# Performance work log

Measured on AMD Instinct MI355X. Metric: run time of the kernel, lower is better.

## Reference

```python
import jax, jax.numpy as jnp
import numpy as np

B, L, D = 8, 4096, 256
G, K = 64, 8          # n_groups, group_size
N = G * K             # 512 slots
H = 8                 # attention heads
EPS = 1e-5

def _ln(x, g, b):
    m = jnp.mean(x, axis=-1, keepdims=True)
    v = jnp.var(x, axis=-1, keepdims=True)
    return (x - m) * jax.lax.rsqrt(v + EPS) * g + b

def _gelu(x):
    return jax.nn.gelu(x, approximate=False)  # torch nn.GELU default = exact erf

def setup_inputs() -> dict:
    key = jax.random.key(0)
    ks = jax.random.split(key, 24)
    s = 0.02
    d = {
        'X': jax.random.normal(ks[0], (B, L, D), jnp.float32),
        'S': jax.random.normal(ks[1], (B, N, D), jnp.float32),
        'Wg':  jax.random.normal(ks[2], (D, G)) * s,
        'Wk':  jax.random.normal(ks[3], (D, K)) * s,
        'Wm1': jax.random.normal(ks[4], (D, 2*D)) * s, 'bm1': jnp.zeros((2*D,)),
        'Wm2': jax.random.normal(ks[5], (2*D, D)) * s, 'bm2': jnp.zeros((D,)),
        'Wgt1': jax.random.normal(ks[6], (D, D)) * s, 'bgt1': jnp.zeros((D,)),
        'Wgt2': jax.random.normal(ks[7], (D, 1)) * s, 'bgt2': jnp.zeros((1,)),
        'Wqkv': jax.random.normal(ks[8], (D, 3*D)) * s, 'bqkv': jnp.zeros((3*D,)),
        'Wo':  jax.random.normal(ks[9], (D, D)) * s, 'bo': jnp.zeros((D,)),
        'aln_g': jnp.ones((D,)), 'aln_b': jnp.zeros((D,)),
        'Wu1': jax.random.normal(ks[10], (2*D, 2*D)) * s, 'bu1': jnp.zeros((2*D,)),
        'Wu2': jax.random.normal(ks[11], (2*D, D)) * s, 'bu2': jnp.zeros((D,)),
        'ln_g': jnp.ones((D,)), 'ln_b': jnp.zeros((D,)),
    }
    return d

def reference(X, S, Wg, Wk, Wm1, bm1, Wm2, bm2, Wgt1, bgt1, Wgt2, bgt2,
              Wqkv, bqkv, Wo, bo, aln_g, aln_b, Wu1, bu1, Wu2, bu2, ln_g, ln_b):
    # --- hierarchical routing (eval path: argmax one-hot) ---
    msg = _gelu(X @ Wm1 + bm1) @ Wm2 + bm2                 # (B,L,D)
    gate = jax.nn.sigmoid(_gelu(X @ Wgt1 + bgt1) @ Wgt2 + bgt2)  # (B,L,1)
    gm = msg * gate
    gidx = jnp.argmax(X @ Wg, axis=-1)                     # (B,L)
    kidx = jnp.argmax(X @ Wk, axis=-1)                     # (B,L)
    idx = gidx * K + kidx                                  # flat slot id in [0,N)
    full = jax.nn.one_hot(idx, N, dtype=X.dtype)           # (B,L,N)
    incoming = jnp.einsum('bln,bld->bnd', full, gm)        # (B,N,D)
    # --- slot self-attention ---
    qkv = S @ Wqkv + bqkv
    q, k, v = jnp.split(qkv, 3, axis=-1)
    dh = D // H
    q = q.reshape(B, N, H, dh); k = k.reshape(B, N, H, dh); v = v.reshape(B, N, H, dh)
    scores = jnp.einsum('bqhd,bkhd->bhqk', q, k) / jnp.sqrt(jnp.asarray(dh, X.dtype))
    attn = jax.nn.softmax(scores, axis=-1)
    o = jnp.einsum('bhqk,bkhd->bqhd', attn, v).reshape(B, N, D) @ Wo + bo
    S1 = _ln(S + o, aln_g, aln_b)
    # --- update ---
    cat = jnp.concatenate([S1, incoming], axis=-1)         # (B,N,2D)
    S2 = S1 + _gelu(cat @ Wu1 + bu1) @ Wu2 + bu2
    return _ln(S2, ln_g, ln_b)
```

## Files before the change

### kernel.cpp

```cpp
#include <hip/hip_runtime.h>

typedef __bf16 bf16_t;
typedef __bf16 bf16x8 __attribute__((ext_vector_type(8)));
typedef __bf16 bf16x4v __attribute__((ext_vector_type(4)));
typedef __bf16 bf16x2v __attribute__((ext_vector_type(2)));
typedef float f32x4 __attribute__((ext_vector_type(4)));
typedef unsigned long long u64;

#define LN_EPS 1e-5f

__device__ __forceinline__ float erf_fast(float a) {
  const float t = fabsf(a);
  const float s = a * a;
  float r;
  if (t > 0.921875f) {
    float u;
    r = fmaf(-1.72853470e-5f, t, 3.83197126e-4f);
    u = fmaf(-3.88396438e-3f, t, 2.42546219e-2f);
    r = fmaf(r, s, u);
    r = fmaf(r, t, 1.06777877e-1f);
    r = fmaf(r, t, -6.37245935e-1f);
    r = fmaf(r, t, -1.28717512e-1f);
    r = fmaf(r, t, t);
    r = 1.0f - __expf(-r);
    r = copysignf(r, a);
  } else {
    r = -5.96761703e-4f;
    r = fmaf(r, s, 4.99119423e-3f);
    r = fmaf(r, s, -2.67681349e-2f);
    r = fmaf(r, s, 1.12819925e-1f);
    r = fmaf(r, s, -3.76125336e-1f);
    r = fmaf(r, s, 1.28379166e-1f);
    r = fmaf(r, a, a);
  }
  return r;
}

__device__ __forceinline__ float gelu_f(float x) {
  const float h = 0.5f * x;
  return fmaf(h, erf_fast(x * 0.70710678118654752f), h);
}

__device__ __forceinline__ void async16(const bf16_t* g, bf16_t* l) {
  __builtin_amdgcn_global_load_lds(
      (const __attribute__((address_space(1))) void*)g,
      (__attribute__((address_space(3))) void*)l, 16, 0, 0);
}

__global__ __launch_bounds__(256)
void prep_kernel(const float* __restrict__ X, const float* __restrict__ S,
                 const float* __restrict__ Wg, const float* __restrict__ Wk,
                 const float* __restrict__ Wm1, const float* __restrict__ Wgt1,
                 const float* __restrict__ Wm2, const float* __restrict__ Wqkv,
                 const float* __restrict__ Wo, const float* __restrict__ Wu1,
                 const float* __restrict__ Wu2,
                 bf16_t* __restrict__ Xb, bf16_t* __restrict__ Sb,
                 bf16_t* __restrict__ W1t, bf16_t* __restrict__ W2t,
                 bf16_t* __restrict__ Wqkvt, bf16_t* __restrict__ Wot,
                 bf16_t* __restrict__ Wu1t, bf16_t* __restrict__ Wu2t,
                 float4* __restrict__ zbase)
{
  const int bid = blockIdx.x;
  const int t = threadIdx.x;
  if (bid < 8192) {
    const int i = bid * 256 + t;
    const float4 v = ((const float4*)X)[i];
    bf16x4v o; o[0]=(bf16_t)v.x; o[1]=(bf16_t)v.y; o[2]=(bf16_t)v.z; o[3]=(bf16_t)v.w;
    ((bf16x4v*)Xb)[i] = o;
  } else if (bid < 9216) {
    const int i = (bid - 8192) * 256 + t;
    const float4 v = ((const float4*)S)[i];
    bf16x4v o; o[0]=(bf16_t)v.x; o[1]=(bf16_t)v.y; o[2]=(bf16_t)v.z; o[3]=(bf16_t)v.w;
    ((bf16x4v*)Sb)[i] = o;
  } else if (bid < 10112) {
    const int n = bid - 9216;
    const int k = t;
    float v;
    if (n < 512)      v = Wm1[k * 512 + n];
    else if (n < 768) v = Wgt1[k * 256 + (n - 512)];
    else if (n < 832) v = Wg[k * 64 + (n - 768)];
    else if (n < 840) v = Wk[k * 8 + (n - 832)];
    else              v = 0.f;
    W1t[n * 256 + k] = (bf16_t)v;
  } else if (bid < 10368) {
    const int n = bid - 10112;
    for (int k = t; k < 512; k += 256) W2t[n * 512 + k] = (bf16_t)Wm2[k * 256 + n];
  } else if (bid < 11136) {
    const int n = bid - 10368;
    Wqkvt[n * 256 + t] = (bf16_t)Wqkv[t * 768 + n];
  } else if (bid < 11392) {
    const int n = bid - 11136;
    Wot[n * 256 + t] = (bf16_t)Wo[t * 256 + n];
  } else if (bid < 11904) {
    const int n = bid - 11392;
    for (int k = t; k < 512; k += 256) Wu1t[n * 512 + k] = (bf16_t)Wu1[k * 512 + n];
  } else if (bid < 12160) {
    const int n = bid - 11904;
    for (int k = t; k < 512; k += 256) Wu2t[n * 512 + k] = (bf16_t)Wu2[k * 256 + n];
  } else {
    zbase[(bid - 12160) * 256 + t] = make_float4(0.f, 0.f, 0.f, 0.f);
  }
}

__global__ __launch_bounds__(256, 2)
void g1_kernel(const bf16_t* __restrict__ A,
               const bf16_t* __restrict__ Bt,
               const float* __restrict__ bias, const float* __restrict__ bias2,
               bf16_t* __restrict__ h1,
               const float* __restrict__ wgt2, float* __restrict__ gatelin,
               u64* __restrict__ bitmap)
{
  const int m0 = blockIdx.x * 128;
  const int by = blockIdx.y;
  const int n0 = by * 128;
  const int t = threadIdx.x;
  const int w = t >> 6;
  const int lane = t & 63;
  const int wr = w >> 1, wc = w & 1;
  const int quad = lane >> 4, l15 = lane & 15;

  __shared__ bf16_t lA[128 * 32];
  __shared__ bf16_t lB[128 * 32];
  __shared__ float sWg[256];
  __shared__ int sKi[128];

  if (by >= 4 && by < 6) sWg[t] = wgt2[t];

  f32x4 acc[4][4];
#pragma unroll
  for (int mt = 0; mt < 4; ++mt)
#pragma unroll
    for (int nt = 0; nt < 4; ++nt)
      acc[mt][nt] = (f32x4){0.f, 0.f, 0.f, 0.f};

  const int srow = t >> 2;
  const int schunk = ((t & 3) ^ (srow & 3)) * 8;
  const int ko = ((quad ^ (l15 & 3)) << 3);

  for (int k0 = 0; k0 < 256; k0 += 32) {
#pragma unroll
    for (int i = 0; i < 2; ++i) {
      const int row = i * 64 + srow;
      async16(A + (size_t)(m0 + row) * 256 + k0 + schunk,
              lA + (size_t)(i * 256 + (t & 192)) * 8);
      async16(Bt + (size_t)(n0 + row) * 256 + k0 + schunk,
              lB + (size_t)(i * 256 + (t & 192)) * 8);
    }
    __syncthreads();
    bf16x8 af[4], bfr[4];
#pragma unroll
    for (int mt = 0; mt < 4; ++mt)
      af[mt] = *(const bf16x8*)&lA[(wr * 64 + mt * 16 + l15) * 32 + ko];
#pragma unroll
    for (int nt = 0; nt < 4; ++nt)
      bfr[nt] = *(const bf16x8*)&lB[(wc * 64 + nt * 16 + l15) * 32 + ko];
#pragma unroll
    for (int mt = 0; mt < 4; ++mt)
#pragma unroll
      for (int nt = 0; nt < 4; ++nt)
        acc[mt][nt] = __builtin_amdgcn_mfma_f32_16x16x32_bf16(bfr[nt], af[mt], acc[mt][nt], 0, 0, 0);
    __syncthreads();
  }

  if (by < 4) {
#pragma unroll
    for (int mt = 0; mt < 4; ++mt) {
      const int row = m0 + wr * 64 + mt * 16 + l15;
#pragma unroll
      for (int nt = 0; nt < 4; ++nt) {
        const int colb = n0 + wc * 64 + nt * 16 + quad * 4;
        const float4 bb = *(const float4*)&bias[colb];
        bf16x4v o;
        o[0] = (bf16_t)gelu_f(acc[mt][nt][0] + bb.x);
        o[1] = (bf16_t)gelu_f(acc[mt][nt][1] + bb.y);
        o[2] = (bf16_t)gelu_f(acc[mt][nt][2] + bb.z);
        o[3] = (bf16_t)gelu_f(acc[mt][nt][3] + bb.w);
        *(bf16x4v*)&h1[(size_t)row * 512 + colb] = o;
      }
    }
  } else if (by < 6) {
#pragma unroll
    for (int mt = 0; mt < 4; ++mt) {
      const int row = m0 + wr * 64 + mt * 16 + l15;
      float part = 0.f;
#pragma unroll
      for (int nt = 0; nt < 4; ++nt) {
        const int colb = n0 + wc * 64 + nt * 16 + quad * 4;
        const int c = colb - 512;
        const float4 bb = *(const float4*)&bias2[c];
        part = fmaf(gelu_f(acc[mt][nt][0] + bb.x), sWg[c + 0], part);
        part = fmaf(gelu_f(acc[mt][nt][1] + bb.y), sWg[c + 1], part);
        part = fmaf(gelu_f(acc[mt][nt][2] + bb.z), sWg[c + 2], part);
        part = fmaf(gelu_f(acc[mt][nt][3] + bb.w), sWg[c + 3], part);
      }
      part += __shfl_xor(part, 16, 64);
      part += __shfl_xor(part, 32, 64);
      if (lane < 16) atomicAdd(&gatelin[row], part);
    }
  } else {
    int bi[4];
#pragma unroll
    for (int mt = 0; mt < 4; ++mt) {
      if (wc == 0) {
        float mv = -1e30f; int mi = 0;
#pragma unroll
        for (int nt = 0; nt < 4; ++nt)
#pragma unroll
          for (int j = 0; j < 4; ++j) {
            const int gc = nt * 16 + quad * 4 + j;
            const float v = acc[mt][nt][j];
            if (v > mv || (v == mv && gc < mi)) { mv = v; mi = gc; }
          }
#pragma unroll
        for (int off = 16; off <= 32; off <<= 1) {
          const float ov = __shfl_xor(mv, off, 64);
          const int oi = __shfl_xor(mi, off, 64);
          if (ov > mv || (ov == mv && oi < mi)) { mv = ov; mi = oi; }
        }
        bi[mt] = mi;
      } else {
        float mv = -1e30f; int mi = 0;
        if (quad < 2) {
#pragma unroll
          for (int j = 0; j < 4; ++j) {
            const int kc = quad * 4 + j;
            const float v = acc[mt][0][j];
            if (v > mv || (v == mv && kc < mi)) { mv = v; mi = kc; }
          }
        }
#pragma unroll
        for (int off = 16; off <= 32; off <<= 1) {
          const float ov = __shfl_xor(mv, off, 64);
          const int oi = __shfl_xor(mi, off, 64);
          if (ov > mv || (ov == mv && oi < mi)) { mv = ov; mi = oi; }
        }
        if (lane < 16) sKi[wr * 64 + mt * 16 + l15] = mi;
      }
    }
    __syncthreads();
    if (wc == 0 && lane < 16) {
#pragma unroll
      for (int mt = 0; mt < 4; ++mt) {
        const int rl = wr * 64 + mt * 16 + l15;
        const int row = m0 + rl;
        const int idx = bi[mt] * 8 + sKi[rl];
        const int b = row >> 12, tok = row & 4095;
        atomicOr(&bitmap[(size_t)(b * 512 + idx) * 64 + (tok >> 6)],
                 1ull << (tok & 63));
      }
    }
  }
}

template<int MT, int EPI>
__global__ __launch_bounds__(256)
void gemm_kernel(const bf16_t* __restrict__ A, int lda,
                 const bf16_t* __restrict__ Bt, int K,
                 const float* __restrict__ bias, const float* __restrict__ bias2,
                 void* __restrict__ outp, int ldc,
                 const float* __restrict__ wgt2, float* __restrict__ gatelin,
                 u64* __restrict__ bitmap)
{
  constexpr int BM = MT * 32;
  constexpr int CA = BM * 4;
  const int m0 = blockIdx.x * BM;
  const int by = blockIdx.y;
  const int n0 = by * 128;
  const int t = threadIdx.x;
  const int w = t >> 6;
  const int lane = t & 63;
  const int wr = w >> 1, wc = w & 1;
  const int quad = lane >> 4, l15 = lane & 15;

  __shared__ bf16_t lA[BM * 32];
  __shared__ bf16_t lB[128 * 32];

  f32x4 acc[MT][4];
#pragma unroll
  for (int mt = 0; mt < MT; ++mt)
#pragma unroll
    for (int nt = 0; nt < 4; ++nt)
      acc[mt][nt] = (f32x4){0.f, 0.f, 0.f, 0.f};

  for (int k0 = 0; k0 < K; k0 += 32) {
    if constexpr (CA >= 256) {
#pragma unroll
      for (int i = 0; i < CA / 256; ++i) {
        const int c = i * 256 + t;
        async16(A + (size_t)(m0 + (c >> 2)) * lda + k0 + (c & 3) * 8,
                lA + (size_t)(i * 256 + (t & 192)) * 8);
      }
    } else {
      if (t < CA)
        async16(A + (size_t)(m0 + (t >> 2)) * lda + k0 + (t & 3) * 8,
                lA + (size_t)(t & 192) * 8);
    }
#pragma unroll
    for (int i = 0; i < 2; ++i) {
      const int c = i * 256 + t;
      async16(Bt + (size_t)(n0 + (c >> 2)) * K + k0 + (c & 3) * 8,
              lB + (size_t)(i * 256 + (t & 192)) * 8);
    }
    __syncthreads();
    bf16x8 af[MT], bfr[4];
    const int ko = quad * 8;
#pragma unroll
    for (int mt = 0; mt < MT; ++mt)
      af[mt] = *(const bf16x8*)&lA[(wr * MT * 16 + mt * 16 + l15) * 32 + ko];
#pragma unroll
    for (int nt = 0; nt < 4; ++nt)
      bfr[nt] = *(const bf16x8*)&lB[(wc * 64 + nt * 16 + l15) * 32 + ko];
#pragma unroll
    for (int mt = 0; mt < MT; ++mt)
#pragma unroll
      for (int nt = 0; nt < 4; ++nt)
        acc[mt][nt] = __builtin_amdgcn_mfma_f32_16x16x32_bf16(bfr[nt], af[mt], acc[mt][nt], 0, 0, 0);
    __syncthreads();
  }

#pragma unroll
  for (int mt = 0; mt < MT; ++mt) {
    const int row = m0 + wr * MT * 16 + mt * 16 + l15;
#pragma unroll
    for (int nt = 0; nt < 4; ++nt) {
      const int colb = n0 + wc * 64 + nt * 16 + quad * 4;
      const float4 bb = *(const float4*)&bias[colb];
      bf16x4v o;
      o[0]=(bf16_t)gelu_f(acc[mt][nt][0]+bb.x); o[1]=(bf16_t)gelu_f(acc[mt][nt][1]+bb.y);
      o[2]=(bf16_t)gelu_f(acc[mt][nt][2]+bb.z); o[3]=(bf16_t)gelu_f(acc[mt][nt][3]+bb.w);
      *(bf16x4v*)&((bf16_t*)outp)[(size_t)row * ldc + colb] = o;
    }
  }
  (void)bias2; (void)wgt2; (void)gatelin; (void)bitmap;
}

__global__ __launch_bounds__(256)
void gemm_pair_kernel(const bf16_t* __restrict__ H, const bf16_t* __restrict__ W2t,
                      const float* __restrict__ bm2, const float* __restrict__ sumg,
                      float* __restrict__ incom,
                      const bf16_t* __restrict__ Sb, const bf16_t* __restrict__ Wqkvt,
                      const float* __restrict__ bqkv, bf16_t* __restrict__ qkvb,
                      bf16_t* __restrict__ Vt)
{
  int id = blockIdx.x;
  const bool first = id < 256;
  if (!first) id -= 256;
  const bf16_t* A  = first ? H : Sb;
  const bf16_t* Bt = first ? W2t : Wqkvt;
  const float* bias = first ? bm2 : bqkv;
  const int lda = first ? 512 : 256;
  const int K   = first ? 512 : 256;
  const int ldc = first ? 256 : 768;
  const int m0 = (id & 127) * 32;
  const int n0 = (id >> 7) * 128;
  const int t = threadIdx.x;
  const int w = t >> 6;
  const int lane = t & 63;
  const int wr = w >> 1, wc = w & 1;
  const int quad = lane >> 4, l15 = lane & 15;

  __shared__ bf16_t lA[32 * 32];
  __shared__ bf16_t lB[128 * 32];

  f32x4 acc[4];
#pragma unroll
  for (int nt = 0; nt < 4; ++nt) acc[nt] = (f32x4){0.f, 0.f, 0.f, 0.f};

  for (int k0 = 0; k0 < K; k0 += 32) {
    if (t < 128)
      async16(A + (size_t)(m0 + (t >> 2)) * lda + k0 + (t & 3) * 8,
              lA + (size_t)(t & 192) * 8);
#pragma unroll
    for (int i = 0; i < 2; ++i) {
      const int c = i * 256 + t;
      async16(Bt + (size_t)(n0 + (c >> 2)) * K + k0 + (c & 3) * 8,
              lB + (size_t)(i * 256 + (t & 192)) * 8);
    }
    __syncthreads();
    bf16x8 af, bfr[4];
    const int ko = quad * 8;
    af = *(const bf16x8*)&lA[(wr * 16 + l15) * 32 + ko];
#pragma unroll
    for (int nt = 0; nt < 4; ++nt)
      bfr[nt] = *(const bf16x8*)&lB[(wc * 64 + nt * 16 + l15) * 32 + ko];
#pragma unroll
    for (int nt = 0; nt < 4; ++nt)
      acc[nt] = __builtin_amdgcn_mfma_f32_16x16x32_bf16(bfr[nt], af, acc[nt], 0, 0, 0);
    __syncthreads();
  }

  const int row = m0 + wr * 16 + l15;
  if (first) {
    const float gt = sumg[row];
#pragma unroll
    for (int nt = 0; nt < 4; ++nt) {
      const int colb = n0 + wc * 64 + nt * 16 + quad * 4;
      const float4 bb = *(const float4*)&bias[colb];
      *(float4*)&incom[(size_t)row * ldc + colb] =
          make_float4(fmaf(gt, bb.x, acc[nt][0]), fmaf(gt, bb.y, acc[nt][1]),
                      fmaf(gt, bb.z, acc[nt][2]), fmaf(gt, bb.w, acc[nt][3]));
    }
  } else if (n0 < 512) {
#pragma unroll
    for (int nt = 0; nt < 4; ++nt) {
      const int colb = n0 + wc * 64 + nt * 16 + quad * 4;
      const float4 bb = *(const float4*)&bias[colb];
      bf16x4v o; o[0]=(bf16_t)(acc[nt][0]+bb.x); o[1]=(bf16_t)(acc[nt][1]+bb.y);
      o[2]=(bf16_t)(acc[nt][2]+bb.z); o[3]=(bf16_t)(acc[nt][3]+bb.w);
      *(bf16x4v*)&qkvb[(size_t)row * ldc + colb] = o;
    }
  } else {
    const int b = row >> 9, key = row & 511;
#pragma unroll
    for (int nt = 0; nt < 4; ++nt) {
      const int colb = n0 + wc * 64 + nt * 16 + quad * 4;
      const int c = colb - 512;
      const int h2 = c >> 5, dh = c & 31;
      const float4 bb = *(const float4*)&bias[colb];
      bf16_t* vb = Vt + ((size_t)(b * 8 + h2) * 32 + dh) * 512 + key;
      vb[0]   = (bf16_t)(acc[nt][0] + bb.x);
      vb[512] = (bf16_t)(acc[nt][1] + bb.y);
      vb[1024]= (bf16_t)(acc[nt][2] + bb.z);
      vb[1536]= (bf16_t)(acc[nt][3] + bb.w);
    }
  }
}

__global__ __launch_bounds__(256)
void gather_kernel(const bf16_t* __restrict__ h1, const float* __restrict__ gatelin,
                   const float* __restrict__ bgt2, const u64* __restrict__ bitmap,
                   bf16_t* __restrict__ H, float* __restrict__ sumg)
{
  const int bs = blockIdx.x;
  const int b = bs >> 9;
  const int t = threadIdx.x;
  __shared__ u64 sw[64];
  if (t < 64) sw[t] = bitmap[(size_t)bs * 64 + t];
  __syncthreads();
  const float bg = bgt2[0];
  float a0 = 0.f, a1 = 0.f, sg = 0.f;
  for (int wd = 0; wd < 64; ++wd) {
    u64 word = sw[wd];
    while (word) {
      const int bit = __builtin_ctzll(word);
      word &= word - 1;
      const int l = (b << 12) + (wd << 6) + bit;
      const float g = 1.0f / (1.0f + __expf(-(gatelin[l] + bg)));
      const bf16x2v hv = *(const bf16x2v*)&h1[(size_t)l * 512 + t * 2];
      a0 = fmaf(g, (float)hv[0], a0);
      a1 = fmaf(g, (float)hv[1], a1);
      sg += g;
    }
  }
  bf16x2v o; o[0] = (bf16_t)a0; o[1] = (bf16_t)a1;
  *(bf16x2v*)&H[(size_t)bs * 512 + t * 2] = o;
  if (t == 0) sumg[bs] = sg;
}

__global__ __launch_bounds__(256)
void attn_kernel(const bf16_t* __restrict__ qkv, const bf16_t* __restrict__ Vt,
                 bf16_t* __restrict__ obuf)
{
  const int bid = blockIdx.x;
  const int qc = bid & 15;
  const int h = (bid >> 4) & 7;
  const int b = bid >> 7;
  const int t = threadIdx.x;
  const int w = t >> 6, lane = t & 63;
  const int quad = lane >> 4, l15 = lane & 15;

  __shared__ bf16_t sP[32 * 520];
  __shared__ float sL[32];

  bf16x8 qf[2];
#pragma unroll
  for (int mt = 0; mt < 2; ++mt) {
    const int row = b * 512 + qc * 32 + mt * 16 + l15;
    qf[mt] = *(const bf16x8*)&qkv[(size_t)row * 768 + h * 32 + quad * 8];
  }
  const float scale = 0.17677669529663687f;
  for (int kt = w; kt < 32; kt += 4) {
    const int key = b * 512 + kt * 16 + l15;
    const bf16x8 kf = *(const bf16x8*)&qkv[(size_t)key * 768 + 256 + h * 32 + quad * 8];
#pragma unroll
    for (int mt = 0; mt < 2; ++mt) {
      f32x4 c = (f32x4){0.f, 0.f, 0.f, 0.f};
      c = __builtin_amdgcn_mfma_f32_16x16x32_bf16(qf[mt], kf, c, 0, 0, 0);
#pragma unroll
      for (int r = 0; r < 4; ++r)
        sP[(mt * 16 + quad * 4 + r) * 520 + kt * 16 + l15] = (bf16_t)(c[r] * scale);
    }
  }
  __syncthreads();

#pragma unroll
  for (int ri = 0; ri < 8; ++ri) {
    const int row = w * 8 + ri;
    const bf16x8 sv = *(const bf16x8*)&sP[row * 520 + lane * 8];
    float sval[8];
    float mx = -1e30f;
#pragma unroll
    for (int j = 0; j < 8; ++j) { sval[j] = (float)sv[j]; mx = fmaxf(mx, sval[j]); }
#pragma unroll
    for (int off = 32; off; off >>= 1) mx = fmaxf(mx, __shfl_xor(mx, off, 64));
    float sum = 0.f;
    bf16x8 pv;
#pragma unroll
    for (int j = 0; j < 8; ++j) { const float e = __expf(sval[j] - mx); sum += e; pv[j] = (bf16_t)e; }
#pragma unroll
    for (int off = 32; off; off >>= 1) sum += __shfl_xor(sum, off, 64);
    *(bf16x8*)&sP[row * 520 + lane * 8] = pv;
    if (lane == 0) sL[row] = sum;
  }
  __syncthreads();

  const int wq = w >> 1, wd = w & 1;
  const bf16_t* vbase = Vt + ((size_t)(b * 8 + h) * 32 + wd * 16 + l15) * 512;
  const bf16_t* pbase = &sP[(wq * 16 + l15) * 520];
  f32x4 oacc = (f32x4){0.f, 0.f, 0.f, 0.f};
#pragma unroll
  for (int kt = 0; kt < 16; ++kt) {
    const bf16x8 af = *(const bf16x8*)&pbase[kt * 32 + quad * 8];
    const bf16x8 vf = *(const bf16x8*)&vbase[kt * 32 + quad * 8];
    oacc = __builtin_amdgcn_mfma_f32_16x16x32_bf16(vf, af, oacc, 0, 0, 0);
  }
  const int rowq = wq * 16 + l15;
  const float inv = 1.0f / sL[rowq];
  bf16x4v o;
#pragma unroll
  for (int r = 0; r < 4; ++r) o[r] = (bf16_t)(oacc[r] * inv);
  *(bf16x4v*)&obuf[(size_t)(b * 512 + qc * 32 + rowq) * 256 + h * 32 + wd * 16 + quad * 4] = o;
}

__global__ __launch_bounds__(256)
void wo_ln1_kernel(const bf16_t* __restrict__ obuf, const bf16_t* __restrict__ Wot,
                   const float* __restrict__ bo, const float* __restrict__ S,
                   const float* __restrict__ incom, const float* __restrict__ g,
                   const float* __restrict__ bb, float* __restrict__ S1f,
                   bf16_t* __restrict__ A4)
{
  const int m0 = blockIdx.x * 16;
  const int t = threadIdx.x;
  const int w = t >> 6, lane = t & 63;
  const int quad = lane >> 4, l15 = lane & 15;

  __shared__ bf16_t lA[16 * 32];
  __shared__ bf16_t lB[256 * 32];
  __shared__ float sSum[4][16];
  __shared__ float sSq[4][16];

  f32x4 acc[4];
#pragma unroll
  for (int nt = 0; nt < 4; ++nt) acc[nt] = (f32x4){0.f, 0.f, 0.f, 0.f};

  for (int k0 = 0; k0 < 256; k0 += 32) {
    if (t < 64)
      async16(obuf + (size_t)(m0 + (t >> 2)) * 256 + k0 + (t & 3) * 8, lA);
#pragma unroll
    for (int i = 0; i < 4; ++i) {
      const int c = i * 256 + t;
      async16(Wot + (size_t)(c >> 2) * 256 + k0 + (c & 3) * 8,
              lB + (size_t)(i * 256 + (t & 192)) * 8);
    }
    __syncthreads();
    const int ko = quad * 8;
    const bf16x8 af = *(const bf16x8*)&lA[l15 * 32 + ko];
#pragma unroll
    for (int nt = 0; nt < 4; ++nt) {
      const bf16x8 bfr = *(const bf16x8*)&lB[(w * 64 + nt * 16 + l15) * 32 + ko];
      acc[nt] = __builtin_amdgcn_mfma_f32_16x16x32_bf16(bfr, af, acc[nt], 0, 0, 0);
    }
    __syncthreads();
  }

  const int row = m0 + l15;
  float sum = 0.f, sq = 0.f;
#pragma unroll
  for (int nt = 0; nt < 4; ++nt) {
    const int colb = w * 64 + nt * 16 + quad * 4;
    const float4 bv = *(const float4*)&bo[colb];
    const float4 sv = *(const float4*)&S[(size_t)row * 256 + colb];
    float x0 = acc[nt][0] + bv.x + sv.x, x1 = acc[nt][1] + bv.y + sv.y;
    float x2 = acc[nt][2] + bv.z + sv.z, x3 = acc[nt][3] + bv.w + sv.w;
    acc[nt][0] = x0; acc[nt][1] = x1; acc[nt][2] = x2; acc[nt][3] = x3;
    sum += x0 + x1 + x2 + x3;
    sq += x0*x0 + x1*x1 + x2*x2 + x3*x3;
  }
  sum += __shfl_xor(sum, 16, 64); sum += __shfl_xor(sum, 32, 64);
  sq  += __shfl_xor(sq, 16, 64);  sq  += __shfl_xor(sq, 32, 64);
  if (lane < 16) { sSum[w][l15] = sum; sSq[w][l15] = sq; }
  __syncthreads();
  const float tot = sSum[0][l15] + sSum[1][l15] + sSum[2][l15] + sSum[3][l15];
  const float tq  = sSq[0][l15] + sSq[1][l15] + sSq[2][l15] + sSq[3][l15];
  const float mean = tot * 0.00390625f;
  const float var = tq * 0.00390625f - mean * mean;
  const float rstd = rsqrtf(var + LN_EPS);
#pragma unroll
  for (int nt = 0; nt < 4; ++nt) {
    const int colb = w * 64 + nt * 16 + quad * 4;
    const float4 gg = *(const float4*)&g[colb];
    const float4 bv = *(const float4*)&bb[colb];
    const float y0 = (acc[nt][0]-mean)*rstd*gg.x + bv.x;
    const float y1 = (acc[nt][1]-mean)*rstd*gg.y + bv.y;
    const float y2 = (acc[nt][2]-mean)*rstd*gg.z + bv.z;
    const float y3 = (acc[nt][3]-mean)*rstd*gg.w + bv.w;
    *(float4*)&S1f[(size_t)row * 256 + colb] = make_float4(y0, y1, y2, y3);
    bf16x4v yb; yb[0]=(bf16_t)y0; yb[1]=(bf16_t)y1; yb[2]=(bf16_t)y2; yb[3]=(bf16_t)y3;
    *(bf16x4v*)&A4[(size_t)row * 512 + colb] = yb;
    const float4 ic = *(const float4*)&incom[(size_t)row * 256 + colb];
    bf16x4v ib; ib[0]=(bf16_t)ic.x; ib[1]=(bf16_t)ic.y; ib[2]=(bf16_t)ic.z; ib[3]=(bf16_t)ic.w;
    *(bf16x4v*)&A4[(size_t)row * 512 + 256 + colb] = ib;
  }
}

__global__ __launch_bounds__(256)
void wu2_ln2_kernel(const bf16_t* __restrict__ U, const bf16_t* __restrict__ Wu2t,
                    const float* __restrict__ bu2, const float* __restrict__ S1f,
                    const float* __restrict__ g, const float* __restrict__ bb,
                    float* __restrict__ out)
{
  const int m0 = blockIdx.x * 16;
  const int t = threadIdx.x;
  const int w = t >> 6, lane = t & 63;
  const int quad = lane >> 4, l15 = lane & 15;

  __shared__ bf16_t lA[16 * 32];
  __shared__ bf16_t lB[256 * 32];
  __shared__ float sSum[4][16];
  __shared__ float sSq[4][16];

  f32x4 acc[4];
#pragma unroll
  for (int nt = 0; nt < 4; ++nt) acc[nt] = (f32x4){0.f, 0.f, 0.f, 0.f};

  for (int k0 = 0; k0 < 512; k0 += 32) {
    if (t < 64)
      async16(U + (size_t)(m0 + (t >> 2)) * 512 + k0 + (t & 3) * 8, lA);
#pragma unroll
    for (int i = 0; i < 4; ++i) {
      const int c = i * 256 + t;
      async16(Wu2t + (size_t)(c >> 2) * 512 + k0 + (c & 3) * 8,
              lB + (size_t)(i * 256 + (t & 192)) * 8);
    }
    __syncthreads();
    const int ko = quad * 8;
    const bf16x8 af = *(const bf16x8*)&lA[l15 * 32 + ko];
#pragma unroll
    for (int nt = 0; nt < 4; ++nt) {
      const bf16x8 bfr = *(const bf16x8*)&lB[(w * 64 + nt * 16 + l15) * 32 + ko];
      acc[nt] = __builtin_amdgcn_mfma_f32_16x16x32_bf16(bfr, af, acc[nt], 0, 0, 0);
    }
    __syncthreads();
  }

  const int row = m0 + l15;
  float sum = 0.f, sq = 0.f;
#pragma unroll
  for (int nt = 0; nt < 4; ++nt) {
    const int colb = w * 64 + nt * 16 + quad * 4;
    const float4 bv = *(const float4*)&bu2[colb];
    const float4 sv = *(const float4*)&S1f[(size_t)row * 256 + colb];
    float x0 = acc[nt][0] + bv.x + sv.x, x1 = acc[nt][1] + bv.y + sv.y;
    float x2 = acc[nt][2] + bv.z + sv.z, x3 = acc[nt][3] + bv.w + sv.w;
    acc[nt][0] = x0; acc[nt][1] = x1; acc[nt][2] = x2; acc[nt][3] = x3;
    sum += x0 + x1 + x2 + x3;
    sq += x0*x0 + x1*x1 + x2*x2 + x3*x3;
  }
  sum += __shfl_xor(sum, 16, 64); sum += __shfl_xor(sum, 32, 64);
  sq  += __shfl_xor(sq, 16, 64);  sq  += __shfl_xor(sq, 32, 64);
  if (lane < 16) { sSum[w][l15] = sum; sSq[w][l15] = sq; }
  __syncthreads();
  const float tot = sSum[0][l15] + sSum[1][l15] + sSum[2][l15] + sSum[3][l15];
  const float tq  = sSq[0][l15] + sSq[1][l15] + sSq[2][l15] + sSq[3][l15];
  const float mean = tot * 0.00390625f;
  const float var = tq * 0.00390625f - mean * mean;
  const float rstd = rsqrtf(var + LN_EPS);
#pragma unroll
  for (int nt = 0; nt < 4; ++nt) {
    const int colb = w * 64 + nt * 16 + quad * 4;
    const float4 gg = *(const float4*)&g[colb];
    const float4 bv = *(const float4*)&bb[colb];
    *(float4*)&out[(size_t)row * 256 + colb] = make_float4(
        (acc[nt][0]-mean)*rstd*gg.x + bv.x, (acc[nt][1]-mean)*rstd*gg.y + bv.y,
        (acc[nt][2]-mean)*rstd*gg.z + bv.z, (acc[nt][3]-mean)*rstd*gg.w + bv.w);
  }
}

extern "C" void kernel_launch(void* const* d_in, const int* in_sizes, int n_in,
                              void* d_out, int out_size, void* d_ws, size_t ws_size,
                              hipStream_t stream)
{
  (void)in_sizes; (void)n_in; (void)out_size; (void)ws_size;
  const float* X    = (const float*)d_in[0];
  const float* S    = (const float*)d_in[1];
  const float* Wg   = (const float*)d_in[2];
  const float* Wk   = (const float*)d_in[3];
  const float* Wm1  = (const float*)d_in[4];
  const float* bm1  = (const float*)d_in[5];
  const float* Wm2  = (const float*)d_in[6];
  const float* bm2  = (const float*)d_in[7];
  const float* Wgt1 = (const float*)d_in[8];
  const float* bgt1 = (const float*)d_in[9];
  const float* Wgt2 = (const float*)d_in[10];
  const float* bgt2 = (const float*)d_in[11];
  const float* Wqkv = (const float*)d_in[12];
  const float* bqkv = (const float*)d_in[13];
  const float* Wo   = (const float*)d_in[14];
  const float* bo   = (const float*)d_in[15];
  const float* alng = (const float*)d_in[16];
  const float* alnb = (const float*)d_in[17];
  const float* Wu1  = (const float*)d_in[18];
  const float* bu1  = (const float*)d_in[19];
  const float* Wu2  = (const float*)d_in[20];
  const float* bu2  = (const float*)d_in[21];
  const float* lng  = (const float*)d_in[22];
  const float* lnb  = (const float*)d_in[23];

  char* p = (char*)d_ws;
  auto carve = [&](size_t bytes) { char* r = p; p += bytes; return r; };
  bf16_t* Xb    = (bf16_t*)carve(16777216);
  bf16_t* Sb    = (bf16_t*)carve(2097152);
  bf16_t* W1t   = (bf16_t*)carve(458752);
  bf16_t* W2t   = (bf16_t*)carve(262144);
  bf16_t* Wqkvt = (bf16_t*)carve(393216);
  bf16_t* Wot   = (bf16_t*)carve(131072);
  bf16_t* Wu1t  = (bf16_t*)carve(524288);
  bf16_t* Wu2t  = (bf16_t*)carve(262144);
  bf16_t* h1    = (bf16_t*)carve(33554432);
  u64*    bitmap  = (u64*)carve(2097152);
  float*  gatelin = (float*)carve(131072);
  float*  incom = (float*)carve(4194304);
  bf16_t* qkvb  = (bf16_t*)carve(6291456);
  bf16_t* Vt    = (bf16_t*)carve(2097152);
  bf16_t* obuf  = (bf16_t*)carve(2097152);
  float*  S1f   = (float*)carve(4194304);
  bf16_t* A4    = (bf16_t*)carve(4194304);
  bf16_t* U     = (bf16_t*)carve(4194304);
  float*  sumg  = (float*)carve(16384);
  bf16_t* H = U;

  prep_kernel<<<12704, 256, 0, stream>>>(X, S, Wg, Wk, Wm1, Wgt1, Wm2, Wqkv, Wo, Wu1, Wu2,
                                         Xb, Sb, W1t, W2t, Wqkvt, Wot, Wu1t, Wu2t,
                                         (float4*)bitmap);
  g1_kernel<<<dim3(256, 7), 256, 0, stream>>>(Xb, W1t, bm1, bgt1, h1,
                                              Wgt2, gatelin, bitmap);
  gather_kernel<<<4096, 256, 0, stream>>>(h1, gatelin, bgt2, bitmap, H, sumg);
  gemm_pair_kernel<<<1024, 256, 0, stream>>>(H, W2t, bm2, sumg, incom,
                                             Sb, Wqkvt, bqkv, qkvb, Vt);
  attn_kernel<<<1024, 256, 0, stream>>>(qkvb, Vt, obuf);
  wo_ln1_kernel<<<256, 256, 0, stream>>>(obuf, Wot, bo, S, incom, alng, alnb, S1f, A4);
  gemm_kernel<2,5><<<dim3(64,4), 256, 0, stream>>>(A4, 512, Wu1t, 512, bu1, nullptr, U, 512,
                                                   nullptr, nullptr, nullptr);
  wu2_ln2_kernel<<<256, 256, 0, stream>>>(U, Wu2t, bu2, S1f, lng, lnb, (float*)d_out);
}
```

Measured before the change: 254.8 us.

## Double-buffer LDS in GEMM kernels and enlarge pair/Wu1 tiles to 128x128

Adds double-buffered shared-memory staging so the async global loads for the next K slice overlap the MFMA work on the current one, with one barrier per slice, in g1, the QKV/W2 pair GEMM and the Wu1 GEMM. The pair and Wu1 GEMMs move from 32- and 64-row tiles to 128x128 tiles with the XOR-swizzled LDS layout, which gives more data reuse per block. The trade-off is far fewer blocks: 256 for the pair kernel and 128 for Wu1 on a GPU with many CUs, which risks leaving compute units idle. It also doubles LDS use per block.

```diff
diff --git a/kernel.cpp b/kernel.cpp
--- a/kernel.cpp
+++ b/kernel.cpp
@@ -119,8 +119,8 @@
   const int wr = w >> 1, wc = w & 1;
   const int quad = lane >> 4, l15 = lane & 15;
 
-  __shared__ bf16_t lA[128 * 32];
-  __shared__ bf16_t lB[128 * 32];
+  __shared__ bf16_t lA[2][128 * 32];
+  __shared__ bf16_t lB[2][128 * 32];
   __shared__ float sWg[256];
   __shared__ int sKi[128];
 
@@ -136,29 +136,40 @@
   const int srow = t >> 2;
   const int schunk = ((t & 3) ^ (srow & 3)) * 8;
   const int ko = ((quad ^ (l15 & 3)) << 3);
-
-  for (int k0 = 0; k0 < 256; k0 += 32) {
+  const int ldst = (t & 192) * 8;
+
+  auto STAGE = [&](int buf, int k0) {
 #pragma unroll
     for (int i = 0; i < 2; ++i) {
       const int row = i * 64 + srow;
-      async16(A + (size_t)(m0 + row) * 256 + k0 + schunk,
-              lA + (size_t)(i * 256 + (t & 192)) * 8);
-      async16(Bt + (size_t)(n0 + row) * 256 + k0 + schunk,
-              lB + (size_t)(i * 256 + (t & 192)) * 8);
-    }
-    __syncthreads();
+      async16(A + (size_t)(m0 + row) * 256 + k0 + schunk, &lA[buf][i * 2048 + ldst]);
+      async16(Bt + (size_t)(n0 + row) * 256 + k0 + schunk, &lB[buf][i * 2048 + ldst]);
+    }
+  };
+  auto COMPUTE = [&](int buf) {
     bf16x8 af[4], bfr[4];
 #pragma unroll
     for (int mt = 0; mt < 4; ++mt)
-      af[mt] = *(const bf16x8*)&lA[(wr * 64 + mt * 16 + l15) * 32 + ko];
+      af[mt] = *(const bf16x8*)&lA[buf][(wr * 64 + mt * 16 + l15) * 32 + ko];
 #pragma unroll
     for (int nt = 0; nt < 4; ++nt)
-      bfr[nt] = *(const bf16x8*)&lB[(wc * 64 + nt * 16 + l15) * 32 + ko];
+      bfr[nt] = *(const bf16x8*)&lB[buf][(wc * 64 + nt * 16 + l15) * 32 + ko];
 #pragma unroll
     for (int mt = 0; mt < 4; ++mt)
 #pragma unroll
       for (int nt = 0; nt < 4; ++nt)
         acc[mt][nt] = __builtin_amdgcn_mfma_f32_16x16x32_bf16(bfr[nt], af[mt], acc[mt][nt], 0, 0, 0);
+  };
+
+  STAGE(0, 0);
+  __syncthreads();
+#pragma unroll
+  for (int k0 = 0; k0 < 256; k0 += 64) {
+    STAGE(1, k0 + 32);
+    COMPUTE(0);
+    __syncthreads();
+    if (k0 + 64 < 256) STAGE(0, k0 + 64);
+    COMPUTE(1);
     __syncthreads();
   }
 
@@ -252,75 +263,191 @@
   }
 }
 
-template<int MT, int EPI>
-__global__ __launch_bounds__(256)
-void gemm_kernel(const bf16_t* __restrict__ A, int lda,
-                 const bf16_t* __restrict__ Bt, int K,
-                 const float* __restrict__ bias, const float* __restrict__ bias2,
-                 void* __restrict__ outp, int ldc,
-                 const float* __restrict__ wgt2, float* __restrict__ gatelin,
-                 u64* __restrict__ bitmap)
-{
-  constexpr int BM = MT * 32;
-  constexpr int CA = BM * 4;
-  const int m0 = blockIdx.x * BM;
-  const int by = blockIdx.y;
-  const int n0 = by * 128;
+__global__ __launch_bounds__(256, 2)
+void pair128_kernel(const bf16_t* __restrict__ H, const bf16_t* __restrict__ W2t,
+                    const float* __restrict__ bm2, const float* __restrict__ sumg,
+                    float* __restrict__ incom,
+                    const bf16_t* __restrict__ Sb, const bf16_t* __restrict__ Wqkvt,
+                    const float* __restrict__ bqkv, bf16_t* __restrict__ qkvb,
+                    bf16_t* __restrict__ Vt)
+{
+  int id = blockIdx.x;
+  const bool first = id < 64;
+  if (!first) id -= 64;
+  const bf16_t* A  = first ? H : Sb;
+  const bf16_t* Bt = first ? W2t : Wqkvt;
+  const float* bias = first ? bm2 : bqkv;
+  const int lda = first ? 512 : 256;
+  const int K   = first ? 512 : 256;
+  const int m0 = (id & 31) * 128;
+  const int n0 = (id >> 5) * 128;
   const int t = threadIdx.x;
   const int w = t >> 6;
   const int lane = t & 63;
   const int wr = w >> 1, wc = w & 1;
   const int quad = lane >> 4, l15 = lane & 15;
 
-  __shared__ bf16_t lA[BM * 32];
-  __shared__ bf16_t lB[128 * 32];
-
-  f32x4 acc[MT][4];
-#pragma unroll
-  for (int mt = 0; mt < MT; ++mt)
+  __shared__ bf16_t lA[2][128 * 32];
+  __shared__ bf16_t lB[2][128 * 32];
+
+  f32x4 acc[4][4];
+#pragma unroll
+  for (int mt = 0; mt < 4; ++mt)
 #pragma unroll
     for (int nt = 0; nt < 4; ++nt)
       acc[mt][nt] = (f32x4){0.f, 0.f, 0.f, 0.f};
 
-  for (int k0 = 0; k0 < K; k0 += 32) {
-    if constexpr (CA >= 256) {
-#pragma unroll
-      for (int i = 0; i < CA / 256; ++i) {
-        const int c = i * 256 + t;
-        async16(A + (size_t)(m0 + (c >> 2)) * lda + k0 + (c & 3) * 8,
-                lA + (size_t)(i * 256 + (t & 192)) * 8);
-      }
-    } else {
-      if (t < CA)
-        async16(A + (size_t)(m0 + (t >> 2)) * lda + k0 + (t & 3) * 8,
-                lA + (size_t)(t & 192) * 8);
-    }
+  const int srow = t >> 2;
+  const int schunk = ((t & 3) ^ (srow & 3)) * 8;
+  const int ko = ((quad ^ (l15 & 3)) << 3);
+  const int ldst = (t & 192) * 8;
+
+  auto STAGE = [&](int buf, int k0) {
 #pragma unroll
     for (int i = 0; i < 2; ++i) {
-      const int c = i * 256 + t;
-      async16(Bt + (size_t)(n0 + (c >> 2)) * K + k0 + (c & 3) * 8,
-              lB + (size_t)(i * 256 + (t & 192)) * 8);
-    }
-    __syncthreads();
-    bf16x8 af[MT], bfr[4];
-    const int ko = quad * 8;
-#pragma unroll
-    for (int mt = 0; mt < MT; ++mt)
-      af[mt] = *(const bf16x8*)&lA[(wr * MT * 16 + mt * 16 + l15) * 32 + ko];
+      const int row = i * 64 + srow;
+      async16(A + (size_t)(m0 + row) * lda + k0 + schunk, &lA[buf][i * 2048 + ldst]);
+      async16(Bt + (size_t)(n0 + row) * K + k0 + schunk, &lB[buf][i * 2048 + ldst]);
+    }
+  };
+  auto COMPUTE = [&](int buf) {
+    bf16x8 af[4], bfr[4];
+#pragma unroll
+    for (int mt = 0; mt < 4; ++mt)
+      af[mt] = *(const bf16x8*)&lA[buf][(wr * 64 + mt * 16 + l15) * 32 + ko];
 #pragma unroll
     for (int nt = 0; nt < 4; ++nt)
-      bfr[nt] = *(const bf16x8*)&lB[(wc * 64 + nt * 16 + l15) * 32 + ko];
-#pragma unroll
-    for (int mt = 0; mt < MT; ++mt)
+      bfr[nt] = *(const bf16x8*)&lB[buf][(wc * 64 + nt * 16 + l15) * 32 + ko];
+#pragma unroll
+    for (int mt = 0; mt < 4; ++mt)
 #pragma unroll
       for (int nt = 0; nt < 4; ++nt)
         acc[mt][nt] = __builtin_amdgcn_mfma_f32_16x16x32_bf16(bfr[nt], af[mt], acc[mt][nt], 0, 0, 0);
-    __syncthreads();
-  }
-
-#pragma unroll
-  for (int mt = 0; mt < MT; ++mt) {
-    const int row = m0 + wr * MT * 16 + mt * 16 + l15;
+  };
+
+  STAGE(0, 0);
+  __syncthreads();
+  for (int k0 = 0; k0 < K; k0 += 64) {
+    STAGE(1, k0 + 32);
+    COMPUTE(0);
+    __syncthreads();
+    if (k0 + 64 < K) STAGE(0, k0 + 64);
+    COMPUTE(1);
+    __syncthreads();
+  }
+
+  if (first) {
+#pragma unroll
+    for (int mt = 0; mt < 4; ++mt) {
+      const int row = m0 + wr * 64 + mt * 16 + l15;
+      const float gt = sumg[row];
+#pragma unroll
+      for (int nt = 0; nt < 4; ++nt) {
+        const int colb = n0 + wc * 64 + nt * 16 + quad * 4;
+        const float4 bb = *(const float4*)&bias[colb];
+        *(float4*)&incom[(size_t)row * 256 + colb] =
+            make_float4(fmaf(gt, bb.x, acc[mt][nt][0]), fmaf(gt, bb.y, acc[mt][nt][1]),
+                        fmaf(gt, bb.z, acc[mt][nt][2]), fmaf(gt, bb.w, acc[mt][nt][3]));
+      }
+    }
+  } else if (n0 < 512) {
+#pragma unroll
+    for (int mt = 0; mt < 4; ++mt) {
+      const int row = m0 + wr * 64 + mt * 16 + l15;
+#pragma unroll
+      for (int nt = 0; nt < 4; ++nt) {
+        const int colb = n0 + wc * 64 + nt * 16 + quad * 4;
+        const float4 bb = *(const float4*)&bias[colb];
+        bf16x4v o; o[0]=(bf16_t)(acc[mt][nt][0]+bb.x); o[1]=(bf16_t)(acc[mt][nt][1]+bb.y);
+        o[2]=(bf16_t)(acc[mt][nt][2]+bb.z); o[3]=(bf16_t)(acc[mt][nt][3]+bb.w);
+        *(bf16x4v*)&qkvb[(size_t)row * 768 + colb] = o;
+      }
+    }
+  } else {
+#pragma unroll
+    for (int mt = 0; mt < 4; ++mt) {
+      const int row = m0 + wr * 64 + mt * 16 + l15;
+      const int b = row >> 9, key = row & 511;
+#pragma unroll
+      for (int nt = 0; nt < 4; ++nt) {
+        const int colb = n0 + wc * 64 + nt * 16 + quad * 4;
+        const int c = colb - 512;
+        const int h2 = c >> 5, dh = c & 31;
+        const float4 bb = *(const float4*)&bias[colb];
+        bf16_t* vb = Vt + ((size_t)(b * 8 + h2) * 32 + dh) * 512 + key;
+        vb[0]   = (bf16_t)(acc[mt][nt][0] + bb.x);
+        vb[512] = (bf16_t)(acc[mt][nt][1] + bb.y);
+        vb[1024]= (bf16_t)(acc[mt][nt][2] + bb.z);
+        vb[1536]= (bf16_t)(acc[mt][nt][3] + bb.w);
+      }
+    }
+  }
+}
+
+__global__ __launch_bounds__(256, 2)
+void g128_gelu_kernel(const bf16_t* __restrict__ A, const bf16_t* __restrict__ Bt,
+                      const float* __restrict__ bias, bf16_t* __restrict__ out)
+{
+  const int m0 = blockIdx.x * 128;
+  const int n0 = blockIdx.y * 128;
+  const int t = threadIdx.x;
+  const int w = t >> 6;
+  const int lane = t & 63;
+  const int wr = w >> 1, wc = w & 1;
+  const int quad = lane >> 4, l15 = lane & 15;
+
+  __shared__ bf16_t lA[2][128 * 32];
+  __shared__ bf16_t lB[2][128 * 32];
+
+  f32x4 acc[4][4];
+#pragma unroll
+  for (int mt = 0; mt < 4; ++mt)
+#pragma unroll
+    for (int nt = 0; nt < 4; ++nt)
+      acc[mt][nt] = (f32x4){0.f, 0.f, 0.f, 0.f};
+
+  const int srow = t >> 2;
+  const int schunk = ((t & 3) ^ (srow & 3)) * 8;
+  const int ko = ((quad ^ (l15 & 3)) << 3);
+  const int ldst = (t & 192) * 8;
+
+  auto STAGE = [&](int buf, int k0) {
+#pragma unroll
+    for (int i = 0; i < 2; ++i) {
+      const int row = i * 64 + srow;
+      async16(A + (size_t)(m0 + row) * 512 + k0 + schunk, &lA[buf][i * 2048 + ldst]);
+      async16(Bt + (size_t)(n0 + row) * 512 + k0 + schunk, &lB[buf][i * 2048 + ldst]);
+    }
+  };
+  auto COMPUTE = [&](int buf) {
+    bf16x8 af[4], bfr[4];
+#pragma unroll
+    for (int mt = 0; mt < 4; ++mt)
+      af[mt] = *(const bf16x8*)&lA[buf][(wr * 64 + mt * 16 + l15) * 32 + ko];
+#pragma unroll
+    for (int nt = 0; nt < 4; ++nt)
+      bfr[nt] = *(const bf16x8*)&lB[buf][(wc * 64 + nt * 16 + l15) * 32 + ko];
+#pragma unroll
+    for (int mt = 0; mt < 4; ++mt)
+#pragma unroll
+      for (int nt = 0; nt < 4; ++nt)
+        acc[mt][nt] = __builtin_amdgcn_mfma_f32_16x16x32_bf16(bfr[nt], af[mt], acc[mt][nt], 0, 0, 0);
+  };
+
+  STAGE(0, 0);
+  __syncthreads();
+  for (int k0 = 0; k0 < 512; k0 += 64) {
+    STAGE(1, k0 + 32);
+    COMPUTE(0);
+    __syncthreads();
+    if (k0 + 64 < 512) STAGE(0, k0 + 64);
+    COMPUTE(1);
+    __syncthreads();
+  }
+
+#pragma unroll
+  for (int mt = 0; mt < 4; ++mt) {
+    const int row = m0 + wr * 64 + mt * 16 + l15;
 #pragma unroll
     for (int nt = 0; nt < 4; ++nt) {
       const int colb = n0 + wc * 64 + nt * 16 + quad * 4;
@@ -328,100 +455,7 @@
       bf16x4v o;
       o[0]=(bf16_t)gelu_f(acc[mt][nt][0]+bb.x); o[1]=(bf16_t)gelu_f(acc[mt][nt][1]+bb.y);
       o[2]=(bf16_t)gelu_f(acc[mt][nt][2]+bb.z); o[3]=(bf16_t)gelu_f(acc[mt][nt][3]+bb.w);
-      *(bf16x4v*)&((bf16_t*)outp)[(size_t)row * ldc + colb] = o;
-    }
-  }
-  (void)bias2; (void)wgt2; (void)gatelin; (void)bitmap;
-}
-
-__global__ __launch_bounds__(256)
-void gemm_pair_kernel(const bf16_t* __restrict__ H, const bf16_t* __restrict__ W2t,
-                      const float* __restrict__ bm2, const float* __restrict__ sumg,
-                      float* __restrict__ incom,
-                      const bf16_t* __restrict__ Sb, const bf16_t* __restrict__ Wqkvt,
-                      const float* __restrict__ bqkv, bf16_t* __restrict__ qkvb,
-                      bf16_t* __restrict__ Vt)
-{
-  int id = blockIdx.x;
-  const bool first = id < 256;
-  if (!first) id -= 256;
-  const bf16_t* A  = first ? H : Sb;
-  const bf16_t* Bt = first ? W2t : Wqkvt;
-  const float* bias = first ? bm2 : bqkv;
-  const int lda = first ? 512 : 256;
-  const int K   = first ? 512 : 256;
-  const int ldc = first ? 256 : 768;
-  const int m0 = (id & 127) * 32;
-  const int n0 = (id >> 7) * 128;
-  const int t = threadIdx.x;
-  const int w = t >> 6;
-  const int lane = t & 63;
-  const int wr = w >> 1, wc = w & 1;
-  const int quad = lane >> 4, l15 = lane & 15;
-
-  __shared__ bf16_t lA[32 * 32];
-  __shared__ bf16_t lB[128 * 32];
-
-  f32x4 acc[4];
-#pragma unroll
-  for (int nt = 0; nt < 4; ++nt) acc[nt] = (f32x4){0.f, 0.f, 0.f, 0.f};
-
-  for (int k0 = 0; k0 < K; k0 += 32) {
-    if (t < 128)
-      async16(A + (size_t)(m0 + (t >> 2)) * lda + k0 + (t & 3) * 8,
-              lA + (size_t)(t & 192) * 8);
-#pragma unroll
-    for (int i = 0; i < 2; ++i) {
-      const int c = i * 256 + t;
-      async16(Bt + (size_t)(n0 + (c >> 2)) * K + k0 + (c & 3) * 8,
-              lB + (size_t)(i * 256 + (t & 192)) * 8);
-    }
-    __syncthreads();
-    bf16x8 af, bfr[4];
-    const int ko = quad * 8;
-    af = *(const bf16x8*)&lA[(wr * 16 + l15) * 32 + ko];
-#pragma unroll
-    for (int nt = 0; nt < 4; ++nt)
-      bfr[nt] = *(const bf16x8*)&lB[(wc * 64 + nt * 16 + l15) * 32 + ko];
-#pragma unroll
-    for (int nt = 0; nt < 4; ++nt)
-      acc[nt] = __builtin_amdgcn_mfma_f32_16x16x32_bf16(bfr[nt], af, acc[nt], 0, 0, 0);
-    __syncthreads();
-  }
-
-  const int row = m0 + wr * 16 + l15;
-  if (first) {
-    const float gt = sumg[row];
-#pragma unroll
-    for (int nt = 0; nt < 4; ++nt) {
-      const int colb = n0 + wc * 64 + nt * 16 + quad * 4;
-      const float4 bb = *(const float4*)&bias[colb];
-      *(float4*)&incom[(size_t)row * ldc + colb] =
-          make_float4(fmaf(gt, bb.x, acc[nt][0]), fmaf(gt, bb.y, acc[nt][1]),
-                      fmaf(gt, bb.z, acc[nt][2]), fmaf(gt, bb.w, acc[nt][3]));
-    }
-  } else if (n0 < 512) {
-#pragma unroll
-    for (int nt = 0; nt < 4; ++nt) {
-      const int colb = n0 + wc * 64 + nt * 16 + quad * 4;
-      const float4 bb = *(const float4*)&bias[colb];
-      bf16x4v o; o[0]=(bf16_t)(acc[nt][0]+bb.x); o[1]=(bf16_t)(acc[nt][1]+bb.y);
-      o[2]=(bf16_t)(acc[nt][2]+bb.z); o[3]=(bf16_t)(acc[nt][3]+bb.w);
-      *(bf16x4v*)&qkvb[(size_t)row * ldc + colb] = o;
-    }
-  } else {
-    const int b = row >> 9, key = row & 511;
-#pragma unroll
-    for (int nt = 0; nt < 4; ++nt) {
-      const int colb = n0 + wc * 64 + nt * 16 + quad * 4;
-      const int c = colb - 512;
-      const int h2 = c >> 5, dh = c & 31;
-      const float4 bb = *(const float4*)&bias[colb];
-      bf16_t* vb = Vt + ((size_t)(b * 8 + h2) * 32 + dh) * 512 + key;
-      vb[0]   = (bf16_t)(acc[nt][0] + bb.x);
-      vb[512] = (bf16_t)(acc[nt][1] + bb.y);
-      vb[1024]= (bf16_t)(acc[nt][2] + bb.z);
-      vb[1536]= (bf16_t)(acc[nt][3] + bb.w);
+      *(bf16x4v*)&out[(size_t)row * 512 + colb] = o;
     }
   }
 }
@@ -745,11 +779,10 @@
   g1_kernel<<<dim3(256, 7), 256, 0, stream>>>(Xb, W1t, bm1, bgt1, h1,
                                               Wgt2, gatelin, bitmap);
   gather_kernel<<<4096, 256, 0, stream>>>(h1, gatelin, bgt2, bitmap, H, sumg);
-  gemm_pair_kernel<<<1024, 256, 0, stream>>>(H, W2t, bm2, sumg, incom,
-                                             Sb, Wqkvt, bqkv, qkvb, Vt);
+  pair128_kernel<<<256, 256, 0, stream>>>(H, W2t, bm2, sumg, incom,
+                                          Sb, Wqkvt, bqkv, qkvb, Vt);
   attn_kernel<<<1024, 256, 0, stream>>>(qkvb, Vt, obuf);
   wo_ln1_kernel<<<256, 256, 0, stream>>>(obuf, Wot, bo, S, incom, alng, alnb, S1f, A4);
-  gemm_kernel<2,5><<<dim3(64,4), 256, 0, stream>>>(A4, 512, Wu1t, 512, bu1, nullptr, U, 512,
-                                                   nullptr, nullptr, nullptr);
+  g128_gelu_kernel<<<dim3(32, 4), 256, 0, stream>>>(A4, Wu1t, bu1, U);
   wu2_ln2_kernel<<<256, 256, 0, stream>>>(U, Wu2t, bu2, S1f, lng, lnb, (float*)d_out);
 }
```

Result: slower. 262.2 us (+2.9%).
